# Kernel tuning notes

Hardware: AMD Instinct MI355X
Metric: run time of the kernel (lower is better)

## Reference

```python
import jax, jax.numpy as jnp
import numpy as np

N = 100000   # nodes
E = 1600000  # edges (before self-loops)
IN = 128     # in_dim
H = 32       # hidden (hardcoded in module)
G = 2048     # graphs in batch
NEG_SLOPE = 0.2  # PyG GATConv default leaky_relu slope


def setup_inputs() -> dict:
    key = jax.random.key(0)
    ks = jax.random.split(key, 20)
    inp = {
        "x": jax.random.normal(ks[0], (N, IN), jnp.float32),
        "edge_index": jax.random.randint(ks[1], (2, E), 0, N, dtype=jnp.int64),
        "batch": jnp.sort(jax.random.randint(ks[2], (N,), 0, G, dtype=jnp.int64)),
    }
    dims = [(IN, H), (H, H), (H, H), (H, H)]
    for i, (di, do) in enumerate(dims, start=1):
        k = 3 + 4 * (i - 1)
        inp[f"W{i}"] = jax.random.normal(ks[k], (di, do), jnp.float32) * 0.1
        inp[f"a_s{i}"] = jax.random.normal(ks[k + 1], (do,), jnp.float32) * 0.1
        inp[f"a_d{i}"] = jax.random.normal(ks[k + 2], (do,), jnp.float32) * 0.1
        inp[f"b{i}"] = jnp.zeros((do,), jnp.float32)
    return inp


def _gat(x, src, dst, W, a_s, a_d, b):
    # PyG GATConv, heads=1: h = xW; e_ij = leaky_relu(a_s.h_j + a_d.h_i);
    # alpha = softmax over incoming edges of i; out_i = sum_j alpha_ij * h_j + b
    h = x @ W                                # [N, H]
    es = h @ a_s                             # [N]
    ed = h @ a_d                             # [N]
    e = jax.nn.leaky_relu(es[src] + ed[dst], NEG_SLOPE)   # [E+N]
    m = jax.ops.segment_max(e, dst, num_segments=N)        # per-dest max (stable softmax)
    ex = jnp.exp(e - m[dst])
    denom = jax.ops.segment_sum(ex, dst, num_segments=N)
    alpha = ex / denom[dst]
    out = jax.ops.segment_sum(alpha[:, None] * h[src], dst, num_segments=N)
    return out + b


def reference(x, edge_index, batch, W1, a_s1, a_d1, b1, W2, a_s2, a_d2, b2,
              W3, a_s3, a_d3, b3, W4, a_s4, a_d4, b4):
    # add self-loops once (GATConv add_self_loops=True; same edge set every layer)
    loop = jnp.arange(N, dtype=edge_index.dtype)
    src = jnp.concatenate([edge_index[0], loop])
    dst = jnp.concatenate([edge_index[1], loop])
    x = _gat(x, src, dst, W1, a_s1, a_d1, b1)  # tanh in source is a no-op (result discarded)
    x = _gat(x, src, dst, W2, a_s2, a_d2, b2)
    x = _gat(x, src, dst, W3, a_s3, a_d3, b3)
    x = _gat(x, src, dst, W4, a_s4, a_d4, b4)
    # global_mean_pool
    sums = jax.ops.segment_sum(x, batch, num_segments=G)
    cnt = jax.ops.segment_sum(jnp.ones((N,), x.dtype), batch, num_segments=G)
    return sums / jnp.maximum(cnt, 1.0)[:, None]
```

## Files before the change

### kernel.cpp

```cpp
#include <hip/hip_runtime.h>
#include <hip/hip_fp16.h>

#define HDIM 32
#define IN_DIM 128
#define NEG_SLOPE 0.2f
#define NPB 128
#define NPB_SHIFT 7
#define MAXB 1024
#define CHUNK 8192
#define CAP 4096

typedef _Float16 half8  __attribute__((ext_vector_type(8)));
typedef _Float16 half4v __attribute__((ext_vector_type(4)));
typedef float    floatx4 __attribute__((ext_vector_type(4)));
typedef float    floatx2 __attribute__((ext_vector_type(2)));

__device__ __forceinline__ float leaky(float e) {
    return (e >= 0.f) ? e : NEG_SLOPE * e;
}


template<int K>
__global__ __launch_bounds__(256) void gemm_mfma(
    const float* __restrict__ x, const float* __restrict__ W,
    const float* __restrict__ a_s, const float* __restrict__ a_d,
    uint2* __restrict__ h8, float* __restrict__ es, float* __restrict__ ed, int N)
{
    constexpr int KP = K + 8;
    __shared__ _Float16 xs[64 * KP];
    __shared__ _Float16 Wt[32 * KP];
    __shared__ float stage[64 * 33];
    const int tid = threadIdx.x;
    for (int i = tid; i < K * 32; i += 256) {
        int k = i >> 5, n = i & 31;
        Wt[n * KP + k] = (_Float16)W[i];
    }
    const int lane = tid & 63;
    const int wave = tid >> 6;
    const int m16  = lane & 15;
    const int quad = lane >> 4;
    const float as0 = a_s[m16], as1 = a_s[m16 + 16];
    const float ad0 = a_d[m16], ad1 = a_d[m16 + 16];

    const int ntiles = (N + 63) >> 6;
    for (int tile = blockIdx.x; tile < ntiles; tile += gridDim.x) {
        const int row0 = tile << 6;
        __syncthreads();
        for (int i = tid; i < 64 * (K / 4); i += 256) {
            int r  = i / (K / 4);
            int c4 = i % (K / 4);
            float4 v = (row0 + r < N) ? ((const float4*)x)[(size_t)(row0 + r) * (K / 4) + c4]
                                      : make_float4(0.f, 0.f, 0.f, 0.f);
            half4v hv = { (_Float16)v.x, (_Float16)v.y, (_Float16)v.z, (_Float16)v.w };
            *(half4v*)&xs[r * KP + c4 * 4] = hv;
        }
        __syncthreads();
        floatx4 acc0 = {0.f, 0.f, 0.f, 0.f}, acc1 = {0.f, 0.f, 0.f, 0.f};
        const int rbase = wave * 16;
        #pragma unroll
        for (int kt = 0; kt < K / 32; kt++) {
            half8 a  = *(half8*)&xs[(rbase + m16) * KP + kt * 32 + quad * 8];
            half8 b0 = *(half8*)&Wt[m16 * KP + kt * 32 + quad * 8];
            half8 b1 = *(half8*)&Wt[(m16 + 16) * KP + kt * 32 + quad * 8];
            acc0 = __builtin_amdgcn_mfma_f32_16x16x32_f16(a, b0, acc0, 0, 0, 0);
            acc1 = __builtin_amdgcn_mfma_f32_16x16x32_f16(a, b1, acc1, 0, 0, 0);
        }
        #pragma unroll
        for (int r = 0; r < 4; r++) {
            const int lr = rbase + quad * 4 + r;
            int row = row0 + lr;
            float c0 = acc0[r], c1 = acc1[r];
            stage[lr * 33 + m16]      = c0;
            stage[lr * 33 + m16 + 16] = c1;
            float ps = c0 * as0 + c1 * as1;
            float pd = c0 * ad0 + c1 * ad1;
            #pragma unroll
            for (int m = 8; m >= 1; m >>= 1) { ps += __shfl_xor(ps, m); pd += __shfl_xor(pd, m); }
            if (row < N && m16 == 0) { es[row] = ps; ed[row] = pd; }
        }
        __syncthreads();
        {
            int r = tid >> 2, seg = tid & 3;
            int row = row0 + r;
            if (row < N) {
                const float* sp = &stage[r * 33 + seg * 8];
                unsigned int u0, u1;
                u0 = __builtin_amdgcn_cvt_pk_fp8_f32(sp[0], sp[1], 0,  false);
                u0 = __builtin_amdgcn_cvt_pk_fp8_f32(sp[2], sp[3], u0, true);
                u1 = __builtin_amdgcn_cvt_pk_fp8_f32(sp[4], sp[5], 0,  false);
                u1 = __builtin_amdgcn_cvt_pk_fp8_f32(sp[6], sp[7], u1, true);
                h8[(size_t)row * 4 + seg] = make_uint2(u0, u1);
            }
        }
    }
}


__global__ __launch_bounds__(256) void chunk_hist(
    const int* __restrict__ dsts, int E, int B, int* __restrict__ cnt2D)
{
    __shared__ int hist[MAXB];
    const int blk = blockIdx.x;
    for (int i = threadIdx.x; i < B; i += 256) hist[i] = 0;
    __syncthreads();
    const int e0 = blk * CHUNK;
    for (int i = threadIdx.x; i < CHUNK; i += 256) {
        int e = e0 + i;
        if (e < E) atomicAdd(&hist[dsts[e] >> NPB_SHIFT], 1);
    }
    __syncthreads();
    for (int i = threadIdx.x; i < B; i += 256) cnt2D[(size_t)blk * B + i] = hist[i];
}

__global__ __launch_bounds__(256) void chunk_scan(
    const int* __restrict__ cnt2D, int NBLK, int B,
    int* __restrict__ off2D, int* __restrict__ bcnt)
{
    __shared__ int s[256];
    const int b = blockIdx.x, t = threadIdx.x;
    int v = (t < NBLK) ? cnt2D[(size_t)t * B + b] : 0;
    s[t] = v;
    __syncthreads();
    for (int off = 1; off < 256; off <<= 1) {
        int add = (t >= off) ? s[t - off] : 0;
        __syncthreads();
        s[t] += add;
        __syncthreads();
    }
    if (t < NBLK) off2D[(size_t)t * B + b] = s[t] - v;
    if (t == 255) bcnt[b] = s[255];
}

__global__ __launch_bounds__(1024) void bucket_scan(
    const int* __restrict__ bcnt, int B, int E,
    int* __restrict__ bstart, int* __restrict__ rowptr, int N)
{
    __shared__ int s[1024];
    const int t = threadIdx.x;
    int v = (t < B) ? bcnt[t] : 0;
    s[t] = v;
    __syncthreads();
    for (int off = 1; off < 1024; off <<= 1) {
        int add = (t >= off) ? s[t - off] : 0;
        __syncthreads();
        s[t] += add;
        __syncthreads();
    }
    if (t < B) bstart[t] = s[t] - v;
    if (t == 0) { bstart[B] = E; rowptr[N] = E; }
}

__global__ __launch_bounds__(256) void pair_scatter2(
    const int* __restrict__ srcs, const int* __restrict__ dsts, int E, int B,
    const int* __restrict__ off2D, const int* __restrict__ bstart,
    int* __restrict__ pairs)
{
    __shared__ int cur[MAXB];
    const int blk = blockIdx.x;
    for (int i = threadIdx.x; i < B; i += 256)
        cur[i] = bstart[i] + off2D[(size_t)blk * B + i];
    __syncthreads();
    const int e0 = blk * CHUNK;
    for (int i = threadIdx.x; i < CHUNK; i += 256) {
        int e = e0 + i;
        if (e < E) {
            int s = srcs[e], d = dsts[e];
            int pos = atomicAdd(&cur[d >> NPB_SHIFT], 1);
            pairs[pos] = (s << NPB_SHIFT) | (d & (NPB - 1));
        }
    }
}

__global__ __launch_bounds__(256) void bucket_sort(
    const int* __restrict__ pairs, const int* __restrict__ bstart,
    int* __restrict__ rowptr, int* __restrict__ csrsrc, int N)
{
    __shared__ int ldeg[NPB];
    __shared__ int lex[NPB];
    __shared__ int recs[CAP];
    __shared__ int sorted[CAP];
    const int b = blockIdx.x, t = threadIdx.x;
    const int p0 = bstart[b], p1 = bstart[b + 1];
    const int cnt = p1 - p0;
    if (t < NPB) ldeg[t] = 0;
    __syncthreads();
    for (int i = t; i < cnt; i += 256) {
        int r = pairs[p0 + i];
        atomicAdd(&ldeg[r & (NPB - 1)], 1);
        if (i < CAP) recs[i] = r;
    }
    __syncthreads();
    if (t < NPB) lex[t] = ldeg[t];
    __syncthreads();
    for (int off = 1; off < NPB; off <<= 1) {
        int add = (t >= off && t < NPB) ? lex[t - off] : 0;
        __syncthreads();
        if (t < NPB) lex[t] += add;
        __syncthreads();
    }
    const int node0 = b * NPB;
    if (t < NPB) {
        int excl = lex[t] - ldeg[t];
        if (node0 + t < N) rowptr[node0 + t] = p0 + excl;
        ldeg[t] = excl;
    }
    __syncthreads();
    if (cnt <= CAP) {
        for (int i = t; i < cnt; i += 256) {
            int r = recs[i];
            int pos = atomicAdd(&ldeg[r & (NPB - 1)], 1);
            sorted[pos] = r >> NPB_SHIFT;
        }
        __syncthreads();
        for (int i = t; i < cnt; i += 256) csrsrc[p0 + i] = sorted[i];
    } else {
        for (int i = t; i < cnt; i += 256) {
            int r = pairs[p0 + i];
            int pos = atomicAdd(&ldeg[r & (NPB - 1)], 1);
            csrsrc[p0 + pos] = r >> NPB_SHIFT;
        }
    }
}


__global__ __launch_bounds__(256) void agg7(
    const uint2* __restrict__ h8, const float* __restrict__ es, const float* __restrict__ ed,
    const int* __restrict__ rowptr, const int* __restrict__ csrsrc,
    const float* __restrict__ b, float* __restrict__ out, int N)
{
    const int gid  = blockIdx.x * 256 + threadIdx.x;
    const int node = gid >> 2;
    const int l    = threadIdx.x & 3;
    if (node >= N) return;

    const int e0 = rowptr[node];
    const int e1 = rowptr[node + 1];
    const float edi = ed[node];

    float a0=0.f,a1=0.f,a2=0.f,a3=0.f,a4=0.f,a5=0.f,a6=0.f,a7=0.f,den=0.f;

    int e = e0;
    for (; e + 8 <= e1; e += 8) {
        int s[8]; float q[8]; uint2 u[8];
        #pragma unroll
        for (int j = 0; j < 8; j++) s[j] = csrsrc[e + j];
        #pragma unroll
        for (int j = 0; j < 8; j++) q[j] = es[s[j]];
        #pragma unroll
        for (int j = 0; j < 8; j++) u[j] = h8[(size_t)s[j] * 4 + l];
        #pragma unroll
        for (int j = 0; j < 8; j++) {
            floatx2 f0 = __builtin_amdgcn_cvt_pk_f32_fp8(u[j].x, false);
            floatx2 f1 = __builtin_amdgcn_cvt_pk_f32_fp8(u[j].x, true);
            floatx2 f2 = __builtin_amdgcn_cvt_pk_f32_fp8(u[j].y, false);
            floatx2 f3 = __builtin_amdgcn_cvt_pk_f32_fp8(u[j].y, true);
            float w = __expf(leaky(q[j] + edi));
            den += w;
            a0 += w*f0.x; a1 += w*f0.y; a2 += w*f1.x; a3 += w*f1.y;
            a4 += w*f2.x; a5 += w*f2.y; a6 += w*f3.x; a7 += w*f3.y;
        }
    }
    for (; e < e1; e++) {
        int s = csrsrc[e];
        float q = es[s];
        uint2 u = h8[(size_t)s * 4 + l];
        floatx2 f0 = __builtin_amdgcn_cvt_pk_f32_fp8(u.x, false);
        floatx2 f1 = __builtin_amdgcn_cvt_pk_f32_fp8(u.x, true);
        floatx2 f2 = __builtin_amdgcn_cvt_pk_f32_fp8(u.y, false);
        floatx2 f3 = __builtin_amdgcn_cvt_pk_f32_fp8(u.y, true);
        float w = __expf(leaky(q + edi));
        den += w;
        a0 += w*f0.x; a1 += w*f0.y; a2 += w*f1.x; a3 += w*f1.y;
        a4 += w*f2.x; a5 += w*f2.y; a6 += w*f3.x; a7 += w*f3.y;
    }
    {
        float w = __expf(leaky(es[node] + edi));
        uint2 u = h8[(size_t)node * 4 + l];
        floatx2 f0 = __builtin_amdgcn_cvt_pk_f32_fp8(u.x, false);
        floatx2 f1 = __builtin_amdgcn_cvt_pk_f32_fp8(u.x, true);
        floatx2 f2 = __builtin_amdgcn_cvt_pk_f32_fp8(u.y, false);
        floatx2 f3 = __builtin_amdgcn_cvt_pk_f32_fp8(u.y, true);
        den += w;
        a0 += w*f0.x; a1 += w*f0.y; a2 += w*f1.x; a3 += w*f1.y;
        a4 += w*f2.x; a5 += w*f2.y; a6 += w*f3.x; a7 += w*f3.y;
    }

    const float4* b4 = (const float4*)b;
    float4 bv0 = b4[2*l], bv1 = b4[2*l + 1];
    float inv = 1.f / den;
    float4 o0, o1;
    o0.x = a0*inv + bv0.x; o0.y = a1*inv + bv0.y; o0.z = a2*inv + bv0.z; o0.w = a3*inv + bv0.w;
    o1.x = a4*inv + bv1.x; o1.y = a5*inv + bv1.y; o1.z = a6*inv + bv1.z; o1.w = a7*inv + bv1.w;
    ((float4*)out)[(size_t)node*8 + 2*l]     = o0;
    ((float4*)out)[(size_t)node*8 + 2*l + 1] = o1;
}


__global__ __launch_bounds__(256) void pool_graph(
    const float* __restrict__ x, const int* __restrict__ batch,
    float* __restrict__ out, int N, int G)
{
    const int g = (blockIdx.x * 256 + threadIdx.x) >> 6;
    if (g >= G) return;
    const int lane = threadIdx.x & 63;
    const int feat = lane & 31;
    const int half = lane >> 5;

    int lo = 0, hi = N;
    while (lo < hi) { int mid = (lo + hi) >> 1; if (batch[mid] < g) lo = mid + 1; else hi = mid; }
    const int start = lo;
    int lo2 = start, hi2 = N;
    while (lo2 < hi2) { int mid = (lo2 + hi2) >> 1; if (batch[mid] < g + 1) lo2 = mid + 1; else hi2 = mid; }
    const int end = lo2;

    float acc = 0.f;
    for (int i = start + half; i < end; i += 2)
        acc += x[(size_t)i * HDIM + feat];
    acc += __shfl_xor(acc, 32);
    if (half == 0) {
        float cnt = (float)(end - start);
        out[(size_t)g * HDIM + feat] = acc / fmaxf(cnt, 1.f);
    }
}


extern "C" void kernel_launch(void* const* d_in, const int* in_sizes, int n_in,
                              void* d_out, int out_size, void* d_ws, size_t ws_size,
                              hipStream_t stream) {
    const float* x          = (const float*)d_in[0];
    const int*   edge_index = (const int*)d_in[1];
    const int*   batch      = (const int*)d_in[2];

    const int N = in_sizes[2];
    const int E = in_sizes[1] / 2;
    const int G = out_size / HDIM;
    const int B = (N + NPB - 1) / NPB;
    const int NBLK = (E + CHUNK - 1) / CHUNK;
    const int ntiles = (N + 63) / 64;

    const int* srcs = edge_index;
    const int* dsts = edge_index + E;

    char* p = (char*)d_ws;
    uint2* h8     = (uint2*)p; p += (size_t)N * 4 * sizeof(uint2);
    float* xbuf   = (float*)p; p += (size_t)N * HDIM * sizeof(float);
    float* es     = (float*)p; p += (size_t)N * sizeof(float);
    float* ed     = (float*)p; p += (size_t)N * sizeof(float);
    int*   rowptr = (int*)p;   p += (size_t)(N + 1) * sizeof(int);
    p += 16 - ((size_t)p & 15);
    int*   csrsrc = (int*)p;   p += (size_t)E * sizeof(int);
    int*   pairs  = (int*)p;   p += (size_t)E * sizeof(int);
    int*   cnt2D  = (int*)p;   p += (size_t)NBLK * B * sizeof(int);
    int*   off2D  = (int*)p;   p += (size_t)NBLK * B * sizeof(int);
    int*   bcnt   = (int*)p;   p += (size_t)B * sizeof(int);
    int*   bstart = (int*)p;   p += (size_t)(B + 1) * sizeof(int);

    chunk_hist  <<<NBLK, 256, 0, stream>>>(dsts, E, B, cnt2D);
    chunk_scan  <<<B, 256, 0, stream>>>(cnt2D, NBLK, B, off2D, bcnt);
    bucket_scan <<<1, 1024, 0, stream>>>(bcnt, B, E, bstart, rowptr, N);
    pair_scatter2<<<NBLK, 256, 0, stream>>>(srcs, dsts, E, B, off2D, bstart, pairs);
    bucket_sort <<<B, 256, 0, stream>>>(pairs, bstart, rowptr, csrsrc, N);

    const int aggGrid = (N * 4 + 255) / 256;

    for (int l = 0; l < 4; l++) {
        const float* W   = (const float*)d_in[3 + 4 * l];
        const float* a_s = (const float*)d_in[4 + 4 * l];
        const float* a_d = (const float*)d_in[5 + 4 * l];
        const float* bb  = (const float*)d_in[6 + 4 * l];

        if (l == 0) gemm_mfma<IN_DIM><<<ntiles, 256, 0, stream>>>(x, W, a_s, a_d, h8, es, ed, N);
        else        gemm_mfma<HDIM>  <<<ntiles, 256, 0, stream>>>(xbuf, W, a_s, a_d, h8, es, ed, N);

        agg7<<<aggGrid, 256, 0, stream>>>(h8, es, ed, rowptr, csrsrc, bb, xbuf, N);
    }

    pool_graph<<<(G * 64 + 255) / 256, 256, 0, stream>>>(xbuf, batch, (float*)d_out, N, G);
}
```

Before: 331.0 us.

## Store intermediate layer outputs in fp16 and use two lanes per node in aggregation

```diff
diff --git a/kernel.cpp b/kernel.cpp
--- a/kernel.cpp
+++ b/kernel.cpp
@@ -21,7 +21,7 @@
 
 
 template<int K>
-__global__ __launch_bounds__(256) void gemm_mfma(
+__global__ __launch_bounds__(256) void gemm_f32in(
     const float* __restrict__ x, const float* __restrict__ W,
     const float* __restrict__ a_s, const float* __restrict__ a_d,
     uint2* __restrict__ h8, float* __restrict__ es, float* __restrict__ ed, int N)
@@ -96,6 +96,84 @@
 }
 
 
+__global__ __launch_bounds__(256) void gemm_f16in(
+    const __half* __restrict__ y, const float* __restrict__ W,
+    const float* __restrict__ a_s, const float* __restrict__ a_d,
+    uint2* __restrict__ h8, float* __restrict__ es, float* __restrict__ ed, int N)
+{
+    constexpr int K = 32, KP = K + 8;
+    __shared__ _Float16 xs[64 * KP];
+    __shared__ _Float16 Wt[32 * KP];
+    __shared__ float stage[64 * 33];
+    const int tid = threadIdx.x;
+    {
+        int i = tid, k = i >> 5, n = i & 31;
+        if (i < K * 32) Wt[n * KP + k] = (_Float16)W[i];
+        i = tid + 256; k = i >> 5; n = i & 31;
+        if (i < K * 32) Wt[n * KP + k] = (_Float16)W[i];
+        i = tid + 512; k = i >> 5; n = i & 31;
+        if (i < K * 32) Wt[n * KP + k] = (_Float16)W[i];
+        i = tid + 768; k = i >> 5; n = i & 31;
+        if (i < K * 32) Wt[n * KP + k] = (_Float16)W[i];
+    }
+    const int lane = tid & 63;
+    const int wave = tid >> 6;
+    const int m16  = lane & 15;
+    const int quad = lane >> 4;
+    const float as0 = a_s[m16], as1 = a_s[m16 + 16];
+    const float ad0 = a_d[m16], ad1 = a_d[m16 + 16];
+
+    const int ntiles = (N + 63) >> 6;
+    for (int tile = blockIdx.x; tile < ntiles; tile += gridDim.x) {
+        const int row0 = tile << 6;
+        __syncthreads();
+        {
+            int r = tid >> 2, c8 = tid & 3;
+            int row = row0 + r;
+            half8 v;
+            if (row < N) v = *(const half8*)((const _Float16*)y + (size_t)row * 32 + c8 * 8);
+            else { v = (half8)(_Float16)0.f; }
+            *(half8*)&xs[r * KP + c8 * 8] = v;
+        }
+        __syncthreads();
+        floatx4 acc0 = {0.f, 0.f, 0.f, 0.f}, acc1 = {0.f, 0.f, 0.f, 0.f};
+        const int rbase = wave * 16;
+        half8 a  = *(half8*)&xs[(rbase + m16) * KP + quad * 8];
+        half8 b0 = *(half8*)&Wt[m16 * KP + quad * 8];
+        half8 b1 = *(half8*)&Wt[(m16 + 16) * KP + quad * 8];
+        acc0 = __builtin_amdgcn_mfma_f32_16x16x32_f16(a, b0, acc0, 0, 0, 0);
+        acc1 = __builtin_amdgcn_mfma_f32_16x16x32_f16(a, b1, acc1, 0, 0, 0);
+        #pragma unroll
+        for (int r = 0; r < 4; r++) {
+            const int lr = rbase + quad * 4 + r;
+            int row = row0 + lr;
+            float c0 = acc0[r], c1 = acc1[r];
+            stage[lr * 33 + m16]      = c0;
+            stage[lr * 33 + m16 + 16] = c1;
+            float ps = c0 * as0 + c1 * as1;
+            float pd = c0 * ad0 + c1 * ad1;
+            #pragma unroll
+            for (int m = 8; m >= 1; m >>= 1) { ps += __shfl_xor(ps, m); pd += __shfl_xor(pd, m); }
+            if (row < N && m16 == 0) { es[row] = ps; ed[row] = pd; }
+        }
+        __syncthreads();
+        {
+            int r = tid >> 2, seg = tid & 3;
+            int row = row0 + r;
+            if (row < N) {
+                const float* sp = &stage[r * 33 + seg * 8];
+                unsigned int u0, u1;
+                u0 = __builtin_amdgcn_cvt_pk_fp8_f32(sp[0], sp[1], 0,  false);
+                u0 = __builtin_amdgcn_cvt_pk_fp8_f32(sp[2], sp[3], u0, true);
+                u1 = __builtin_amdgcn_cvt_pk_fp8_f32(sp[4], sp[5], 0,  false);
+                u1 = __builtin_amdgcn_cvt_pk_fp8_f32(sp[6], sp[7], u1, true);
+                h8[(size_t)row * 4 + seg] = make_uint2(u0, u1);
+            }
+        }
+    }
+}
+
+
 __global__ __launch_bounds__(256) void chunk_hist(
     const int* __restrict__ dsts, int E, int B, int* __restrict__ cnt2D)
 {
@@ -223,76 +301,99 @@
 }
 
 
-__global__ __launch_bounds__(256) void agg7(
-    const uint2* __restrict__ h8, const float* __restrict__ es, const float* __restrict__ ed,
+__device__ __forceinline__ void acc16(float* acc, uint4 u, float w) {
+    floatx2 f0 = __builtin_amdgcn_cvt_pk_f32_fp8(u.x, false);
+    floatx2 f1 = __builtin_amdgcn_cvt_pk_f32_fp8(u.x, true);
+    floatx2 f2 = __builtin_amdgcn_cvt_pk_f32_fp8(u.y, false);
+    floatx2 f3 = __builtin_amdgcn_cvt_pk_f32_fp8(u.y, true);
+    floatx2 f4 = __builtin_amdgcn_cvt_pk_f32_fp8(u.z, false);
+    floatx2 f5 = __builtin_amdgcn_cvt_pk_f32_fp8(u.z, true);
+    floatx2 f6 = __builtin_amdgcn_cvt_pk_f32_fp8(u.w, false);
+    floatx2 f7 = __builtin_amdgcn_cvt_pk_f32_fp8(u.w, true);
+    acc[0]  += w * f0.x; acc[1]  += w * f0.y; acc[2]  += w * f1.x; acc[3]  += w * f1.y;
+    acc[4]  += w * f2.x; acc[5]  += w * f2.y; acc[6]  += w * f3.x; acc[7]  += w * f3.y;
+    acc[8]  += w * f4.x; acc[9]  += w * f4.y; acc[10] += w * f5.x; acc[11] += w * f5.y;
+    acc[12] += w * f6.x; acc[13] += w * f6.y; acc[14] += w * f7.x; acc[15] += w * f7.y;
+}
+
+template<bool LAST>
+__global__ __launch_bounds__(256) void agg8(
+    const uint4* __restrict__ h8, const float* __restrict__ es, const float* __restrict__ ed,
     const int* __restrict__ rowptr, const int* __restrict__ csrsrc,
-    const float* __restrict__ b, float* __restrict__ out, int N)
+    const float* __restrict__ b, __half* __restrict__ y16, float* __restrict__ out, int N)
 {
     const int gid  = blockIdx.x * 256 + threadIdx.x;
-    const int node = gid >> 2;
-    const int l    = threadIdx.x & 3;
+    const int node = gid >> 1;
+    const int l    = threadIdx.x & 1;
     if (node >= N) return;
 
     const int e0 = rowptr[node];
     const int e1 = rowptr[node + 1];
     const float edi = ed[node];
 
-    float a0=0.f,a1=0.f,a2=0.f,a3=0.f,a4=0.f,a5=0.f,a6=0.f,a7=0.f,den=0.f;
+    float acc[16];
+    #pragma unroll
+    for (int i = 0; i < 16; i++) acc[i] = 0.f;
+    float den = 0.f;
 
     int e = e0;
     for (; e + 8 <= e1; e += 8) {
-        int s[8]; float q[8]; uint2 u[8];
+        int s[8]; float q[8]; uint4 u[8];
         #pragma unroll
         for (int j = 0; j < 8; j++) s[j] = csrsrc[e + j];
         #pragma unroll
         for (int j = 0; j < 8; j++) q[j] = es[s[j]];
         #pragma unroll
-        for (int j = 0; j < 8; j++) u[j] = h8[(size_t)s[j] * 4 + l];
+        for (int j = 0; j < 8; j++) u[j] = h8[(size_t)s[j] * 2 + l];
         #pragma unroll
         for (int j = 0; j < 8; j++) {
-            floatx2 f0 = __builtin_amdgcn_cvt_pk_f32_fp8(u[j].x, false);
-            floatx2 f1 = __builtin_amdgcn_cvt_pk_f32_fp8(u[j].x, true);
-            floatx2 f2 = __builtin_amdgcn_cvt_pk_f32_fp8(u[j].y, false);
-            floatx2 f3 = __builtin_amdgcn_cvt_pk_f32_fp8(u[j].y, true);
             float w = __expf(leaky(q[j] + edi));
             den += w;
-            a0 += w*f0.x; a1 += w*f0.y; a2 += w*f1.x; a3 += w*f1.y;
-            a4 += w*f2.x; a5 += w*f2.y; a6 += w*f3.x; a7 += w*f3.y;
+            acc16(acc, u[j], w);
         }
     }
     for (; e < e1; e++) {
         int s = csrsrc[e];
-        float q = es[s];
-        uint2 u = h8[(size_t)s * 4 + l];
-        floatx2 f0 = __builtin_amdgcn_cvt_pk_f32_fp8(u.x, false);
-        floatx2 f1 = __builtin_amdgcn_cvt_pk_f32_fp8(u.x, true);
-        floatx2 f2 = __builtin_amdgcn_cvt_pk_f32_fp8(u.y, false);
-        floatx2 f3 = __builtin_amdgcn_cvt_pk_f32_fp8(u.y, true);
-        float w = __expf(leaky(q + edi));
+        float w = __expf(leaky(es[s] + edi));
+        uint4 u = h8[(size_t)s * 2 + l];
         den += w;
-        a0 += w*f0.x; a1 += w*f0.y; a2 += w*f1.x; a3 += w*f1.y;
-        a4 += w*f2.x; a5 += w*f2.y; a6 += w*f3.x; a7 += w*f3.y;
+        acc16(acc, u, w);
     }
     {
         float w = __expf(leaky(es[node] + edi));
-        uint2 u = h8[(size_t)node * 4 + l];
-        floatx2 f0 = __builtin_amdgcn_cvt_pk_f32_fp8(u.x, false);
-        floatx2 f1 = __builtin_amdgcn_cvt_pk_f32_fp8(u.x, true);
-        floatx2 f2 = __builtin_amdgcn_cvt_pk_f32_fp8(u.y, false);
-        floatx2 f3 = __builtin_amdgcn_cvt_pk_f32_fp8(u.y, true);
+        uint4 u = h8[(size_t)node * 2 + l];
         den += w;
-        a0 += w*f0.x; a1 += w*f0.y; a2 += w*f1.x; a3 += w*f1.y;
-        a4 += w*f2.x; a5 += w*f2.y; a6 += w*f3.x; a7 += w*f3.y;
+        acc16(acc, u, w);
     }
 
     const float4* b4 = (const float4*)b;
-    float4 bv0 = b4[2*l], bv1 = b4[2*l + 1];
     float inv = 1.f / den;
-    float4 o0, o1;
-    o0.x = a0*inv + bv0.x; o0.y = a1*inv + bv0.y; o0.z = a2*inv + bv0.z; o0.w = a3*inv + bv0.w;
-    o1.x = a4*inv + bv1.x; o1.y = a5*inv + bv1.y; o1.z = a6*inv + bv1.z; o1.w = a7*inv + bv1.w;
-    ((float4*)out)[(size_t)node*8 + 2*l]     = o0;
-    ((float4*)out)[(size_t)node*8 + 2*l + 1] = o1;
+    float o[16];
+    #pragma unroll
+    for (int g = 0; g < 4; g++) {
+        float4 bv = b4[l * 4 + g];
+        o[g*4+0] = acc[g*4+0] * inv + bv.x;
+        o[g*4+1] = acc[g*4+1] * inv + bv.y;
+        o[g*4+2] = acc[g*4+2] * inv + bv.z;
+        o[g*4+3] = acc[g*4+3] * inv + bv.w;
+    }
+
+    if (LAST) {
+        float4* op = (float4*)out + (size_t)node * 8 + l * 4;
+        #pragma unroll
+        for (int g = 0; g < 4; g++) {
+            float4 v = { o[g*4+0], o[g*4+1], o[g*4+2], o[g*4+3] };
+            op[g] = v;
+        }
+    } else {
+        _Float16* yp = (_Float16*)y16 + (size_t)node * 32 + l * 16;
+        half8 v0 = { (_Float16)o[0], (_Float16)o[1], (_Float16)o[2], (_Float16)o[3],
+                     (_Float16)o[4], (_Float16)o[5], (_Float16)o[6], (_Float16)o[7] };
+        half8 v1 = { (_Float16)o[8], (_Float16)o[9], (_Float16)o[10], (_Float16)o[11],
+                     (_Float16)o[12], (_Float16)o[13], (_Float16)o[14], (_Float16)o[15] };
+        *(half8*)yp = v0;
+        *(half8*)(yp + 8) = v1;
+    }
 }
 
 
@@ -343,6 +444,7 @@
 
     char* p = (char*)d_ws;
     uint2* h8     = (uint2*)p; p += (size_t)N * 4 * sizeof(uint2);
+    __half* y16   = (__half*)p; p += (size_t)N * HDIM * sizeof(__half);
     float* xbuf   = (float*)p; p += (size_t)N * HDIM * sizeof(float);
     float* es     = (float*)p; p += (size_t)N * sizeof(float);
     float* ed     = (float*)p; p += (size_t)N * sizeof(float);
@@ -361,7 +463,7 @@
     pair_scatter2<<<NBLK, 256, 0, stream>>>(srcs, dsts, E, B, off2D, bstart, pairs);
     bucket_sort <<<B, 256, 0, stream>>>(pairs, bstart, rowptr, csrsrc, N);
 
-    const int aggGrid = (N * 4 + 255) / 256;
+    const int aggGrid = (N * 2 + 255) / 256;
 
     for (int l = 0; l < 4; l++) {
         const float* W   = (const float*)d_in[3 + 4 * l];
@@ -369,10 +471,11 @@
         const float* a_d = (const float*)d_in[5 + 4 * l];
         const float* bb  = (const float*)d_in[6 + 4 * l];
 
-        if (l == 0) gemm_mfma<IN_DIM><<<ntiles, 256, 0, stream>>>(x, W, a_s, a_d, h8, es, ed, N);
-        else        gemm_mfma<HDIM>  <<<ntiles, 256, 0, stream>>>(xbuf, W, a_s, a_d, h8, es, ed, N);
-
-        agg7<<<aggGrid, 256, 0, stream>>>(h8, es, ed, rowptr, csrsrc, bb, xbuf, N);
+        if (l == 0) gemm_f32in<IN_DIM><<<ntiles, 256, 0, stream>>>(x, W, a_s, a_d, h8, es, ed, N);
+        else        gemm_f16in<<<ntiles, 256, 0, stream>>>(y16, W, a_s, a_d, h8, es, ed, N);
+
+        if (l < 3)  agg8<false><<<aggGrid, 256, 0, stream>>>((const uint4*)h8, es, ed, rowptr, csrsrc, bb, y16, xbuf, N);
+        else        agg8<true> <<<aggGrid, 256, 0, stream>>>((const uint4*)h8, es, ed, rowptr, csrsrc, bb, y16, xbuf, N);
     }
 
     pool_graph<<<(G * 64 + 255) / 256, 256, 0, stream>>>(xbuf, batch, (float*)d_out, N, G);
```

Result: no change. 333.4 us (+0.7%).
